# Kernel optimization log

Measured on AMD Instinct MI355X. Metric: run time of the kernel, lower is better.

The kernel has to match this reference:

```python
import jax, jax.numpy as jnp
import numpy as np

RANK = 256
ORDER = 3
B = 8192
NODES_PER = 9
NMAP = 5 ** 6          # 15625 dnn-key nodes
NDD = NMAP + 1         # + 1 device node
MDD = 2048             # edges into device node
POW5 = jnp.array([5**5, 5**4, 5**3, 5**2, 5, 1], dtype=jnp.int32)


def sage_gcn(x, src, dst, n, W, b):
    # DGL SAGEConv(aggregator='gcn'): h = fc((sum_in_neighbors + self) / (in_deg + 1))
    agg = jax.ops.segment_sum(x[src], dst, num_segments=n)
    deg = jax.ops.segment_sum(jnp.ones((src.shape[0],), x.dtype), dst, num_segments=n)
    h = (agg + x) / (deg + 1.0)[:, None]
    return h @ W + b


def layernorm(x, g, b, eps=1e-5):
    m = x.mean(-1, keepdims=True)
    v = ((x - m) ** 2).mean(-1, keepdims=True)
    return (x - m) * jax.lax.rsqrt(v + eps) * g + b


def setup_inputs() -> dict:
    key = jax.random.key(0)
    ks = jax.random.split(key, 10)
    rng = np.random.default_rng(0)
    # batched DNN graphs: B bidirectional 9-node chains
    base = np.arange(B, dtype=np.int32)[:, None] * NODES_PER
    s = (base + np.arange(NODES_PER - 1, dtype=np.int32)[None, :]).ravel()
    d = s + 1
    edge_src = jnp.asarray(np.concatenate([s, d]))
    edge_dst = jnp.asarray(np.concatenate([d, s]))
    # unique key tuples (base-5 digits of unique dnn indices)
    key_idx = rng.choice(NMAP, size=B, replace=False).astype(np.int32)
    digits = np.stack([(key_idx // 5 ** (5 - j)) % 5 for j in range(6)], axis=1)
    key_ids = jnp.asarray(digits, dtype=jnp.int32)
    features = jax.random.randint(ks[0], (B, NODES_PER), 0, 6, dtype=jnp.int32)
    dd_src = jnp.asarray(rng.choice(NMAP, size=MDD, replace=False).astype(np.int32))

    r = RANK
    def gn(k, shape, scale=0.02):
        return jax.random.normal(k, shape, jnp.float32) * scale

    return dict(
        features=features, key_ids=key_ids,
        edge_src=edge_src, edge_dst=edge_dst, dd_src=dd_src,
        emb=gn(ks[1], (6, r)),
        sage_W=gn(ks[2], (ORDER, r, r)), sage_b=jnp.zeros((ORDER, r)),
        ln_g=jnp.ones((ORDER, r)), ln_b=jnp.zeros((ORDER, r)),
        dd_W=gn(ks[3], (r, r)), dd_b=jnp.zeros((r,)),
        norm_g=jnp.ones((r,)), norm_b=jnp.zeros((r,)),
        info_W=gn(ks[4], (5, r)), info_b=jnp.zeros((r,)),
        aug_data=gn(ks[5], (1, 5), 1.0),
        pred_W1=gn(ks[6], (2 * r, r)), pred_b1=jnp.zeros((r,)),
        pred_W2=gn(ks[7], (r, 1)), pred_b2=jnp.zeros((1,)),
    )


def reference(features, key_ids, edge_src, edge_dst, dd_src,
              emb, sage_W, sage_b, ln_g, ln_b,
              dd_W, dd_b, norm_g, norm_b,
              info_W, info_b, aug_data,
              pred_W1, pred_b1, pred_W2, pred_b2):
    n = B * NODES_PER
    # GraphReader: embed + ORDER x (SAGEConv-gcn -> LayerNorm -> ReLU)
    feats = emb[features].reshape(n, RANK)
    for i in range(ORDER):
        feats = sage_gcn(feats, edge_src, edge_dst, n, sage_W[i], sage_b[i])
        feats = jax.nn.relu(layernorm(feats, ln_g[i], ln_b[i]))
    # first node of each 9-node sub-graph
    graph_embeds = feats.reshape(B, NODES_PER, RANK)[:, 0]  # [B, r]

    # scatter graph embeddings into the dnn-device graph node features
    key_idx = (key_ids * POW5).sum(axis=1)  # base-5 index from 6-tuple
    dd = jnp.zeros((NDD, RANK), feats.dtype).at[key_idx].set(graph_embeds)
    info = aug_data @ info_W + info_b  # [1, r]
    dd = dd.at[NDD - 1].set(info[0])

    # SAGEConv-gcn on the dnn-device graph (all edges point at the device node)
    dd_dst = jnp.full_like(dd_src, NDD - 1)
    dd = sage_gcn(dd, dd_src, dd_dst, NDD, dd_W, dd_b)
    dd = jax.nn.relu(layernorm(dd, norm_g, norm_b))

    info_embeds = jnp.broadcast_to(dd[-1], (B, RANK))
    embeds = jnp.concatenate([graph_embeds, info_embeds], axis=1)  # [B, 2r]
    h = jax.nn.relu(embeds @ pred_W1 + pred_b1)
    return h @ pred_W2 + pred_b2  # [B, 1]
```

## Files before the change

### kernel.cpp

```cpp
#include <hip/hip_runtime.h>

#define RANK 256
#define NB 8192
#define NMAP 15625

typedef unsigned short ushort_t;
typedef short  mfma_ab __attribute__((ext_vector_type(8)));
typedef float  f32x4   __attribute__((ext_vector_type(4)));

#define GEH_OFF   0
#define GEL_OFF   4194304
#define WTH_OFF   8388608
#define WTL_OFF   8912896
#define INV_OFF   9437184
#define PARTS_OFF 9499712
#define C2_OFF    9630784

#define DD_BLOCKS 128

__device__ __forceinline__ float b2f(ushort_t u) {
    return __uint_as_float(((unsigned)u) << 16);
}
__device__ __forceinline__ ushort_t f2b(float f) {
    unsigned u = __float_as_uint(f);
    return (ushort_t)((u + 0x7FFFu + ((u >> 16) & 1u)) >> 16);
}

__device__ __forceinline__ f32x4 mfma_bf16(mfma_ab a, mfma_ab b, f32x4 c) {
#if defined(__gfx950__)
    return __builtin_amdgcn_mfma_f32_16x16x32_bf16(a, b, c, 0, 0, 0);
#else
    (void)a; (void)b;
    return c;
#endif
}

__global__ void k_init_inv(int* inv) {
    int i = blockIdx.x * 256 + threadIdx.x;
    if (i < NMAP) inv[i] = -1;
}

__global__ void k_scatter(const int* key_ids, int* inv) {
    int b = blockIdx.x * 256 + threadIdx.x;
    const int* kp = key_ids + b * 6;
    int k = kp[0]*3125 + kp[1]*625 + kp[2]*125 + kp[3]*25 + kp[4]*5 + kp[5];
    inv[k] = b;
}

__global__ void k_prep_w(const float* __restrict__ sageW,
                         const float* __restrict__ predW1,
                         ushort_t* __restrict__ WTh,
                         ushort_t* __restrict__ WTl)
{
    const int id = blockIdx.x;
    const int mat = id >> 4, tile = id & 15;
    const int tr = tile >> 2, tc = tile & 3;
    const float* src = (mat < 3) ? (sageW + mat * 65536) : predW1;
    ushort_t* dh = WTh + mat * 65536;
    ushort_t* dl = WTl + mat * 65536;
    __shared__ float t[64][65];
    const int tid = threadIdx.x;
    const int c = tid & 63, r0 = tid >> 6;
    #pragma unroll
    for (int i = 0; i < 16; ++i) {
        int r = r0 + i * 4;
        t[r][c] = src[(tr*64 + r) * 256 + tc*64 + c];
    }
    __syncthreads();
    #pragma unroll
    for (int i = 0; i < 16; ++i) {
        int r = r0 + i * 4;
        float f = t[c][r];
        ushort_t h = f2b(f);
        dh[(tc*64 + r) * 256 + tr*64 + c] = h;
        dl[(tc*64 + r) * 256 + tr*64 + c] = f2b(f - b2f(h));
    }
}

#define GR_G 3
#define GR_RPAD 32
#define XP 260
#define AP 264

#define LN_PART(ACC0, ACC1, MT)                                                \
    _Pragma("unroll")                                                          \
    for (int q = 0; q < 4; ++q) {                                              \
        ACC0[q] += bias0; ACC1[q] += bias1;                                    \
        float s_  = ACC0[q] + ACC1[q];                                         \
        float ss_ = ACC0[q] * ACC0[q] + ACC1[q] * ACC1[q];                     \
        _Pragma("unroll")                                                      \
        for (int mask = 1; mask <= 8; mask <<= 1) {                            \
            s_  += __shfl_xor(s_, mask, 64);                                   \
            ss_ += __shfl_xor(ss_, mask, 64);                                  \
        }                                                                      \
        if (l15 == 0) sPart[(MT) * 16 + q4 * 4 + q][wid] = make_float2(s_, ss_);\
    }

#define LN_WRITE(ACC0, ACC1, MT)                                               \
    _Pragma("unroll")                                                          \
    for (int q = 0; q < 4; ++q) {                                              \
        const int row_ = (MT) * 16 + q4 * 4 + q;                               \
        if (row_ < nreal) {                                                    \
            const float2 mr_ = sMV[row_];                                      \
            float v0_ = (ACC0[q] - mr_.x) * mr_.y * gv0 + bv0;                 \
            float v1_ = (ACC1[q] - mr_.x) * mr_.y * gv1 + bv1;                 \
            v0_ = fmaxf(v0_, 0.f); v1_ = fmaxf(v1_, 0.f);                      \
            if (L < 2) {                                                       \
                sXf[row_ * XP + colb + l15]      = v0_;                        \
                sXf[row_ * XP + colb + 16 + l15] = v1_;                        \
            } else if ((row_ % 9) == 0) {                                      \
                const int gi_ = row_ / 9;                                      \
                const ushort_t h0_ = f2b(v0_), h1_ = f2b(v1_);                 \
                GEh[(b0 + gi_) * RANK + colb + l15]      = h0_;                \
                GEl[(b0 + gi_) * RANK + colb + l15]      = f2b(v0_ - b2f(h0_));\
                GEh[(b0 + gi_) * RANK + colb + 16 + l15] = h1_;                \
                GEl[(b0 + gi_) * RANK + colb + 16 + l15] = f2b(v1_ - b2f(h1_));\
            }                                                                  \
        }                                                                      \
    }

__global__ __launch_bounds__(512, 4) void k_graph_reader(
    const int* __restrict__ features,
    const float* __restrict__ emb,
    const ushort_t* __restrict__ WTh,
    const ushort_t* __restrict__ WTl,
    const float* __restrict__ sageB,
    const float* __restrict__ lnG,
    const float* __restrict__ lnB,
    ushort_t* __restrict__ GEh,
    ushort_t* __restrict__ GEl)
{
    __shared__ __align__(16) float    sXf[27 * XP];
    __shared__ __align__(16) ushort_t sAh[GR_RPAD * AP];
    __shared__ __align__(16) ushort_t sAl[GR_RPAD * AP];
    __shared__ float2 sPart[GR_RPAD][8];
    __shared__ float2 sMV[GR_RPAD];
    __shared__ int sFeat[GR_RPAD];

    const int tid  = threadIdx.x;
    const int wid  = tid >> 6;
    const int lane = tid & 63;
    const int q4   = lane >> 4;
    const int l15  = lane & 15;
    const int colb = wid * 32;

    const int b0    = blockIdx.x * GR_G;
    const int ngr   = min(GR_G, NB - b0);
    const int nreal = ngr * 9;
    const int ntask = nreal * 64;

    if (tid < GR_RPAD) sFeat[tid] = (tid < nreal) ? features[b0 * 9 + tid] : 0;
    __syncthreads();

    #pragma unroll
    for (int it = 0; it < 4; ++it) {
        int t = tid + it * 512;
        if (t < ntask) {
            int row = t >> 6, c4 = t & 63;
            *(float4*)(sXf + row * XP + c4 * 4) =
                *(const float4*)(emb + sFeat[row] * RANK + c4 * 4);
        }
    }

    const f32x4 vzero = {0.f, 0.f, 0.f, 0.f};

    for (int L = 0; L < 3; ++L) {
        float bias0, bias1, gv0, gv1, bv0, bv1;
        {
            int col0 = colb + l15, col1 = colb + 16 + l15;
            bias0 = sageB[L * RANK + col0]; bias1 = sageB[L * RANK + col1];
            gv0   = lnG[L * RANK + col0];   gv1   = lnG[L * RANK + col1];
            bv0   = lnB[L * RANK + col0];   bv1   = lnB[L * RANK + col1];
        }
        __syncthreads();

        #pragma unroll
        for (int it = 0; it < 4; ++it) {
            int t = tid + it * 512;
            if (t < ntask) {
                int row = t >> 6, c4 = t & 63;
                int j = row % 9;
                float4 v = *(const float4*)(sXf + row * XP + c4 * 4);
                float cnt = 1.f;
                if (j > 0) {
                    float4 u = *(const float4*)(sXf + (row - 1) * XP + c4 * 4);
                    v.x += u.x; v.y += u.y; v.z += u.z; v.w += u.w; cnt += 1.f;
                }
                if (j < 8) {
                    float4 u = *(const float4*)(sXf + (row + 1) * XP + c4 * 4);
                    v.x += u.x; v.y += u.y; v.z += u.z; v.w += u.w; cnt += 1.f;
                }
                float sc = 1.0f / cnt;
                v.x *= sc; v.y *= sc; v.z *= sc; v.w *= sc;
                ushort_t h0 = f2b(v.x), h1 = f2b(v.y), h2 = f2b(v.z), h3 = f2b(v.w);
                ushort_t l0 = f2b(v.x - b2f(h0)), l1 = f2b(v.y - b2f(h1));
                ushort_t l2 = f2b(v.z - b2f(h2)), l3 = f2b(v.w - b2f(h3));
                *(uint2*)(sAh + row * AP + c4 * 4) =
                    make_uint2((unsigned)h0 | ((unsigned)h1 << 16),
                               (unsigned)h2 | ((unsigned)h3 << 16));
                *(uint2*)(sAl + row * AP + c4 * 4) =
                    make_uint2((unsigned)l0 | ((unsigned)l1 << 16),
                               (unsigned)l2 | ((unsigned)l3 << 16));
            }
        }
        __syncthreads();

        f32x4 acc00 = vzero, acc01 = vzero, acc10 = vzero, acc11 = vzero;
        const ushort_t* bh = WTh + L * 65536 + (colb + l15) * RANK + q4 * 8;
        const ushort_t* bl = WTl + L * 65536 + (colb + l15) * RANK + q4 * 8;
        #pragma unroll
        for (int ks = 0; ks < 8; ++ks) {
            mfma_ab B0h = *(const mfma_ab*)(bh + ks * 32);
            mfma_ab B0l = *(const mfma_ab*)(bl + ks * 32);
            mfma_ab B1h = *(const mfma_ab*)(bh + 16 * RANK + ks * 32);
            mfma_ab B1l = *(const mfma_ab*)(bl + 16 * RANK + ks * 32);
            const int ab = l15 * AP + ks * 32 + q4 * 8;

            mfma_ab A0h = *(const mfma_ab*)(sAh + ab);
            mfma_ab A0l = *(const mfma_ab*)(sAl + ab);
            acc00 = mfma_bf16(A0h, B0h, acc00);
            acc00 = mfma_bf16(A0l, B0h, acc00);
            acc00 = mfma_bf16(A0h, B0l, acc00);
            acc01 = mfma_bf16(A0h, B1h, acc01);
            acc01 = mfma_bf16(A0l, B1h, acc01);
            acc01 = mfma_bf16(A0h, B1l, acc01);

            mfma_ab A1h = *(const mfma_ab*)(sAh + ab + 16 * AP);
            mfma_ab A1l = *(const mfma_ab*)(sAl + ab + 16 * AP);
            acc10 = mfma_bf16(A1h, B0h, acc10);
            acc10 = mfma_bf16(A1l, B0h, acc10);
            acc10 = mfma_bf16(A1h, B0l, acc10);
            acc11 = mfma_bf16(A1h, B1h, acc11);
            acc11 = mfma_bf16(A1l, B1h, acc11);
            acc11 = mfma_bf16(A1h, B1l, acc11);
        }

        LN_PART(acc00, acc01, 0)
        LN_PART(acc10, acc11, 1)
        __syncthreads();

        if (tid < GR_RPAD) {
            float s = 0.f, q = 0.f;
            #pragma unroll
            for (int w = 0; w < 8; ++w) { float2 p = sPart[tid][w]; s += p.x; q += p.y; }
            float m = s * (1.0f / 256.0f);
            float var = q * (1.0f / 256.0f) - m * m;
            if (var < 0.f) var = 0.f;
            sMV[tid] = make_float2(m, rsqrtf(var + 1e-5f));
        }
        __syncthreads();

        LN_WRITE(acc00, acc01, 0)
        LN_WRITE(acc10, acc11, 1)
    }
}

__global__ void k_dd_agg(const int* __restrict__ dd_src,
                         const int* __restrict__ inv,
                         const ushort_t* __restrict__ GEh,
                         const ushort_t* __restrict__ GEl,
                         float* __restrict__ parts)
{
    const int c  = threadIdx.x;
    const int e0 = blockIdx.x * (2048 / DD_BLOCKS);
    float s = 0.f;
    for (int e = e0; e < e0 + (2048 / DD_BLOCKS); ++e) {
        int b = inv[dd_src[e]];
        if (b >= 0) s += b2f(GEh[b * RANK + c]) + b2f(GEl[b * RANK + c]);
    }
    parts[blockIdx.x * RANK + c] = s;
}

__global__ void k_device(const float* __restrict__ parts,
                         const float* __restrict__ aug,
                         const float* __restrict__ infoW,
                         const float* __restrict__ infoB,
                         const float* __restrict__ ddW,
                         const float* __restrict__ ddB,
                         const float* __restrict__ normG,
                         const float* __restrict__ normB,
                         const float* __restrict__ predW1,
                         const float* __restrict__ predB1,
                         float* __restrict__ c2)
{
    __shared__ float sh[RANK];
    __shared__ float sdev[RANK];
    __shared__ float sred[RANK];
    const int n = threadIdx.x;

    float agg = 0.f;
    for (int p = 0; p < DD_BLOCKS; ++p) agg += parts[p * RANK + n];
    float info = infoB[n];
    for (int j = 0; j < 5; ++j) info += aug[j] * infoW[j * RANK + n];
    sh[n] = (agg + info) * (1.0f / 2049.0f);
    __syncthreads();

    float y = ddB[n];
    for (int k = 0; k < RANK; ++k) y += sh[k] * ddW[k * RANK + n];

    sred[n] = y; __syncthreads();
    for (int off = 128; off > 0; off >>= 1) {
        if (n < off) sred[n] += sred[n + off];
        __syncthreads();
    }
    float s = sred[0]; __syncthreads();
    sred[n] = y * y; __syncthreads();
    for (int off = 128; off > 0; off >>= 1) {
        if (n < off) sred[n] += sred[n + off];
        __syncthreads();
    }
    float q = sred[0]; __syncthreads();

    float m = s * (1.0f / 256.0f);
    float var = q * (1.0f / 256.0f) - m * m;
    if (var < 0.f) var = 0.f;
    float rs = rsqrtf(var + 1e-5f);
    float dev = (y - m) * rs * normG[n] + normB[n];
    if (dev < 0.f) dev = 0.f;
    sdev[n] = dev;
    __syncthreads();

    float o = predB1[n];
    for (int k = 0; k < RANK; ++k) o += sdev[k] * predW1[(RANK + k) * RANK + n];
    c2[n] = o;
}

#define PRED_MFMA3(ACC, AH, AL, BH, BL)                                        \
    ACC = mfma_bf16(AH, BH, ACC);                                              \
    ACC = mfma_bf16(AL, BH, ACC);                                              \
    ACC = mfma_bf16(AH, BL, ACC);

#define PRED_N(NT, C0, C1)                                                     \
    {                                                                          \
        mfma_ab Bh_ = *(const mfma_ab*)(bh + (NT) * 16 * RANK + ks * 32);      \
        mfma_ab Bl_ = *(const mfma_ab*)(bl + (NT) * 16 * RANK + ks * 32);      \
        PRED_MFMA3(C0, A0h, A0l, Bh_, Bl_)                                     \
        PRED_MFMA3(C1, A1h, A1l, Bh_, Bl_)                                     \
    }

#define PRED_EPI(NT, C0, C1)                                                   \
    {                                                                          \
        const int col_ = colb + (NT) * 16 + l15;                               \
        const float c2v_ = c2[col_], w2v_ = predW2[col_];                      \
        op00 += fmaxf(C0[0] + c2v_, 0.f) * w2v_;                               \
        op01 += fmaxf(C0[1] + c2v_, 0.f) * w2v_;                               \
        op02 += fmaxf(C0[2] + c2v_, 0.f) * w2v_;                               \
        op03 += fmaxf(C0[3] + c2v_, 0.f) * w2v_;                               \
        op10 += fmaxf(C1[0] + c2v_, 0.f) * w2v_;                               \
        op11 += fmaxf(C1[1] + c2v_, 0.f) * w2v_;                               \
        op12 += fmaxf(C1[2] + c2v_, 0.f) * w2v_;                               \
        op13 += fmaxf(C1[3] + c2v_, 0.f) * w2v_;                               \
    }

__global__ __launch_bounds__(128, 4) void k_pred(
    const ushort_t* __restrict__ GEh,
    const ushort_t* __restrict__ GEl,
    const ushort_t* __restrict__ W1h,
    const ushort_t* __restrict__ W1l,
    const float* __restrict__ c2,
    const float* __restrict__ predW2,
    const float* __restrict__ predB2,
    float* __restrict__ out)
{
    __shared__ float sO[2][32];
    const int tid = threadIdx.x;
    const int wid = tid >> 6;
    const int lane = tid & 63;
    const int q4 = lane >> 4, l15 = lane & 15;
    const int colb = wid * 128;
    const int m0 = blockIdx.x * 32;

    const f32x4 vzero = {0.f, 0.f, 0.f, 0.f};
    f32x4 c00 = vzero, c01 = vzero, c02 = vzero, c03 = vzero;
    f32x4 c04 = vzero, c05 = vzero, c06 = vzero, c07 = vzero;
    f32x4 c10 = vzero, c11 = vzero, c12 = vzero, c13 = vzero;
    f32x4 c14 = vzero, c15 = vzero, c16 = vzero, c17 = vzero;

    const ushort_t* ah0 = GEh + (m0 + l15) * RANK + q4 * 8;
    const ushort_t* al0 = GEl + (m0 + l15) * RANK + q4 * 8;
    const ushort_t* ah1 = ah0 + 16 * RANK;
    const ushort_t* al1 = al0 + 16 * RANK;
    const ushort_t* bh = W1h + (colb + l15) * RANK + q4 * 8;
    const ushort_t* bl = W1l + (colb + l15) * RANK + q4 * 8;

    #pragma unroll
    for (int ks = 0; ks < 8; ++ks) {
        mfma_ab A0h = *(const mfma_ab*)(ah0 + ks * 32);
        mfma_ab A0l = *(const mfma_ab*)(al0 + ks * 32);
        mfma_ab A1h = *(const mfma_ab*)(ah1 + ks * 32);
        mfma_ab A1l = *(const mfma_ab*)(al1 + ks * 32);
        PRED_N(0, c00, c10) PRED_N(1, c01, c11)
        PRED_N(2, c02, c12) PRED_N(3, c03, c13)
        PRED_N(4, c04, c14) PRED_N(5, c05, c15)
        PRED_N(6, c06, c16) PRED_N(7, c07, c17)
    }

    float op00 = 0.f, op01 = 0.f, op02 = 0.f, op03 = 0.f;
    float op10 = 0.f, op11 = 0.f, op12 = 0.f, op13 = 0.f;
    PRED_EPI(0, c00, c10) PRED_EPI(1, c01, c11)
    PRED_EPI(2, c02, c12) PRED_EPI(3, c03, c13)
    PRED_EPI(4, c04, c14) PRED_EPI(5, c05, c15)
    PRED_EPI(6, c06, c16) PRED_EPI(7, c07, c17)

    #pragma unroll
    for (int mask = 1; mask <= 8; mask <<= 1) {
        op00 += __shfl_xor(op00, mask, 64); op01 += __shfl_xor(op01, mask, 64);
        op02 += __shfl_xor(op02, mask, 64); op03 += __shfl_xor(op03, mask, 64);
        op10 += __shfl_xor(op10, mask, 64); op11 += __shfl_xor(op11, mask, 64);
        op12 += __shfl_xor(op12, mask, 64); op13 += __shfl_xor(op13, mask, 64);
    }
    if (l15 == 0) {
        sO[wid][q4 * 4 + 0] = op00; sO[wid][q4 * 4 + 1] = op01;
        sO[wid][q4 * 4 + 2] = op02; sO[wid][q4 * 4 + 3] = op03;
        sO[wid][16 + q4 * 4 + 0] = op10; sO[wid][16 + q4 * 4 + 1] = op11;
        sO[wid][16 + q4 * 4 + 2] = op12; sO[wid][16 + q4 * 4 + 3] = op13;
    }
    __syncthreads();
    if (tid < 32) out[m0 + tid] = sO[0][tid] + sO[1][tid] + predB2[0];
}

extern "C" void kernel_launch(void* const* d_in, const int* in_sizes, int n_in,
                              void* d_out, int out_size, void* d_ws, size_t ws_size,
                              hipStream_t stream) {
    const int* features  = (const int*)d_in[0];
    const int* key_ids   = (const int*)d_in[1];
    const int* dd_src    = (const int*)d_in[4];
    const float* emb     = (const float*)d_in[5];
    const float* sageW   = (const float*)d_in[6];
    const float* sageB   = (const float*)d_in[7];
    const float* lnG     = (const float*)d_in[8];
    const float* lnB     = (const float*)d_in[9];
    const float* ddW     = (const float*)d_in[10];
    const float* ddB     = (const float*)d_in[11];
    const float* normG   = (const float*)d_in[12];
    const float* normB   = (const float*)d_in[13];
    const float* infoW   = (const float*)d_in[14];
    const float* infoB   = (const float*)d_in[15];
    const float* aug     = (const float*)d_in[16];
    const float* predW1  = (const float*)d_in[17];
    const float* predB1  = (const float*)d_in[18];
    const float* predW2  = (const float*)d_in[19];
    const float* predB2  = (const float*)d_in[20];

    char* ws = (char*)d_ws;
    ushort_t* GEh   = (ushort_t*)(ws + GEH_OFF);
    ushort_t* GEl   = (ushort_t*)(ws + GEL_OFF);
    ushort_t* WTh   = (ushort_t*)(ws + WTH_OFF);
    ushort_t* WTl   = (ushort_t*)(ws + WTL_OFF);
    int*      inv   = (int*)(ws + INV_OFF);
    float*    parts = (float*)(ws + PARTS_OFF);
    float*    c2    = (float*)(ws + C2_OFF);
    float*    outp  = (float*)d_out;

    k_init_inv<<<62, 256, 0, stream>>>(inv);
    k_scatter<<<32, 256, 0, stream>>>(key_ids, inv);
    k_prep_w<<<64, 256, 0, stream>>>(sageW, predW1, WTh, WTl);
    k_graph_reader<<<(NB + GR_G - 1) / GR_G, 512, 0, stream>>>(
        features, emb, WTh, WTl, sageB, lnG, lnB, GEh, GEl);
    k_dd_agg<<<DD_BLOCKS, 256, 0, stream>>>(dd_src, inv, GEh, GEl, parts);
    k_device<<<1, 256, 0, stream>>>(parts, aug, infoW, infoB, ddW, ddB,
                                    normG, normB, predW1, predB1, c2);
    k_pred<<<NB / 32, 128, 0, stream>>>(GEh, GEl, WTh + 3 * 65536, WTl + 3 * 65536,
                                        c2, predW2, predB2, outp);
}
```

Before: 436.4 us.

## Apply neighbour aggregation after the GEMM via register shuffles, pack 5 graphs per block

Uses linearity to reorder the SAGE layer: the 256x256 matmul is applied to the raw features and the 3-point chain stencil (mean of self and neighbours) is then applied to the MFMA accumulators through cross-lane shuffles. This removes the separate shared-memory stencil pass, its fp32 staging buffer and one barrier per layer. Block size grows from 3 to 5 graphs (45 rows padded to 48, three 16-row M tiles) so each B-fragment load feeds more MFMAs, and B fragments are prefetched one k-step ahead. The bf16 hi/lo split is now applied before the stencil, so rounding behaviour changes slightly, and per-thread register pressure rises.

```diff
diff --git a/kernel.cpp b/kernel.cpp
--- a/kernel.cpp
+++ b/kernel.cpp
@@ -33,6 +33,14 @@
     (void)a; (void)b;
     return c;
 #endif
+}
+
+__device__ __forceinline__ float sten1(float x, float up, float dn, int R) {
+    int j = R % 9;
+    float fu = (j != 0) ? 1.f : 0.f;
+    float fd = (j != 8) ? 1.f : 0.f;
+    float sc = (fu + fd > 1.5f) ? (1.f / 3.f) : 0.5f;
+    return (x + fu * up + fd * dn) * sc;
 }
 
 __global__ void k_init_inv(int* inv) {
@@ -77,9 +85,9 @@
     }
 }
 
-#define GR_G 3
-#define GR_RPAD 32
-#define XP 260
+#define GR_G 5
+#define GR_ROWS 45
+#define GR_RPAD 48
 #define AP 264
 
 #define LN_PART(ACC0, ACC1, MT)                                                \
@@ -93,7 +101,9 @@
             s_  += __shfl_xor(s_, mask, 64);                                   \
             ss_ += __shfl_xor(ss_, mask, 64);                                  \
         }                                                                      \
-        if (l15 == 0) sPart[(MT) * 16 + q4 * 4 + q][wid] = make_float2(s_, ss_);\
+        const int prow_ = (MT) * 16 + q4 * 4 + q;                              \
+        if (l15 == 0 && prow_ < GR_ROWS)                                       \
+            sPart[prow_][wid] = make_float2(s_, ss_);                          \
     }
 
 #define LN_WRITE(ACC0, ACC1, MT)                                               \
@@ -105,18 +115,55 @@
             float v0_ = (ACC0[q] - mr_.x) * mr_.y * gv0 + bv0;                 \
             float v1_ = (ACC1[q] - mr_.x) * mr_.y * gv1 + bv1;                 \
             v0_ = fmaxf(v0_, 0.f); v1_ = fmaxf(v1_, 0.f);                      \
+            const ushort_t h0_ = f2b(v0_), h1_ = f2b(v1_);                     \
+            const ushort_t lo0_ = f2b(v0_ - b2f(h0_));                         \
+            const ushort_t lo1_ = f2b(v1_ - b2f(h1_));                         \
             if (L < 2) {                                                       \
-                sXf[row_ * XP + colb + l15]      = v0_;                        \
-                sXf[row_ * XP + colb + 16 + l15] = v1_;                        \
+                sXh[row_ * AP + colb + l15]      = h0_;                        \
+                sXl[row_ * AP + colb + l15]      = lo0_;                       \
+                sXh[row_ * AP + colb + 16 + l15] = h1_;                        \
+                sXl[row_ * AP + colb + 16 + l15] = lo1_;                       \
             } else if ((row_ % 9) == 0) {                                      \
                 const int gi_ = row_ / 9;                                      \
-                const ushort_t h0_ = f2b(v0_), h1_ = f2b(v1_);                 \
                 GEh[(b0 + gi_) * RANK + colb + l15]      = h0_;                \
-                GEl[(b0 + gi_) * RANK + colb + l15]      = f2b(v0_ - b2f(h0_));\
+                GEl[(b0 + gi_) * RANK + colb + l15]      = lo0_;               \
                 GEh[(b0 + gi_) * RANK + colb + 16 + l15] = h1_;                \
-                GEl[(b0 + gi_) * RANK + colb + 16 + l15] = f2b(v1_ - b2f(h1_));\
+                GEl[(b0 + gi_) * RANK + colb + 16 + l15] = lo1_;               \
             }                                                                  \
         }                                                                      \
+    }
+
+#define STENCIL_COL(V0, V1, V2)                                                \
+    {                                                                          \
+        float ui0 = __shfl(V0[3], lane - 16), di0 = __shfl(V0[0], lane + 16);  \
+        float ui1 = __shfl(V1[3], lane - 16), di1 = __shfl(V1[0], lane + 16);  \
+        float ui2 = __shfl(V2[3], lane - 16), di2 = __shfl(V2[0], lane + 16);  \
+        float xu1 = __shfl(V0[3], l15 + 48);       \
+        float xu2 = __shfl(V1[3], l15 + 48);       \
+        float xd0 = __shfl(V1[0], l15);           \
+        float xd1 = __shfl(V2[0], l15);           \
+        const int rb0 = q4 * 4, rb1 = 16 + q4 * 4, rb2 = 32 + q4 * 4;          \
+        float u0 = (q4 == 0) ? 0.f : ui0;                                      \
+        float d0 = (q4 == 3) ? xd0 : di0;                                      \
+        float u1 = (q4 == 0) ? xu1 : ui1;                                      \
+        float d1 = (q4 == 3) ? xd1 : di1;                                      \
+        float u2 = (q4 == 0) ? xu2 : ui2;                                      \
+        float d2 = (q4 == 3) ? 0.f : di2;                                      \
+        float z00 = sten1(V0[0], u0,    V0[1], rb0 + 0);                       \
+        float z01 = sten1(V0[1], V0[0], V0[2], rb0 + 1);                       \
+        float z02 = sten1(V0[2], V0[1], V0[3], rb0 + 2);                       \
+        float z03 = sten1(V0[3], V0[2], d0,    rb0 + 3);                       \
+        float z10 = sten1(V1[0], u1,    V1[1], rb1 + 0);                       \
+        float z11 = sten1(V1[1], V1[0], V1[2], rb1 + 1);                       \
+        float z12 = sten1(V1[2], V1[1], V1[3], rb1 + 2);                       \
+        float z13 = sten1(V1[3], V1[2], d1,    rb1 + 3);                       \
+        float z20 = sten1(V2[0], u2,    V2[1], rb2 + 0);                       \
+        float z21 = sten1(V2[1], V2[0], V2[2], rb2 + 1);                       \
+        float z22 = sten1(V2[2], V2[1], V2[3], rb2 + 2);                       \
+        float z23 = sten1(V2[3], V2[2], d2,    rb2 + 3);                       \
+        V0[0] = z00; V0[1] = z01; V0[2] = z02; V0[3] = z03;                    \
+        V1[0] = z10; V1[1] = z11; V1[2] = z12; V1[3] = z13;                    \
+        V2[0] = z20; V2[1] = z21; V2[2] = z22; V2[3] = z23;                    \
     }
 
 __global__ __launch_bounds__(512, 4) void k_graph_reader(
@@ -130,12 +177,11 @@
     ushort_t* __restrict__ GEh,
     ushort_t* __restrict__ GEl)
 {
-    __shared__ __align__(16) float    sXf[27 * XP];
-    __shared__ __align__(16) ushort_t sAh[GR_RPAD * AP];
-    __shared__ __align__(16) ushort_t sAl[GR_RPAD * AP];
-    __shared__ float2 sPart[GR_RPAD][8];
-    __shared__ float2 sMV[GR_RPAD];
-    __shared__ int sFeat[GR_RPAD];
+    __shared__ __align__(16) ushort_t sXh[GR_RPAD * AP];
+    __shared__ __align__(16) ushort_t sXl[GR_RPAD * AP];
+    __shared__ float2 sPart[GR_ROWS][8];
+    __shared__ float2 sMV[GR_ROWS];
+    __shared__ int sFeat[GR_ROWS];
 
     const int tid  = threadIdx.x;
     const int wid  = tid >> 6;
@@ -147,19 +193,26 @@
     const int b0    = blockIdx.x * GR_G;
     const int ngr   = min(GR_G, NB - b0);
     const int nreal = ngr * 9;
-    const int ntask = nreal * 64;
-
-    if (tid < GR_RPAD) sFeat[tid] = (tid < nreal) ? features[b0 * 9 + tid] : 0;
+
+    if (tid < GR_ROWS) sFeat[tid] = (tid < nreal) ? features[b0 * 9 + tid] : 0;
     __syncthreads();
 
     #pragma unroll
-    for (int it = 0; it < 4; ++it) {
+    for (int it = 0; it < 6; ++it) {
         int t = tid + it * 512;
-        if (t < ntask) {
-            int row = t >> 6, c4 = t & 63;
-            *(float4*)(sXf + row * XP + c4 * 4) =
-                *(const float4*)(emb + sFeat[row] * RANK + c4 * 4);
-        }
+        int row = t >> 6, c4 = t & 63;
+        float4 v = make_float4(0.f, 0.f, 0.f, 0.f);
+        if (row < nreal)
+            v = *(const float4*)(emb + sFeat[row] * RANK + c4 * 4);
+        ushort_t h0 = f2b(v.x), h1 = f2b(v.y), h2 = f2b(v.z), h3 = f2b(v.w);
+        ushort_t l0 = f2b(v.x - b2f(h0)), l1 = f2b(v.y - b2f(h1));
+        ushort_t l2 = f2b(v.z - b2f(h2)), l3 = f2b(v.w - b2f(h3));
+        *(uint2*)(sXh + row * AP + c4 * 4) =
+            make_uint2((unsigned)h0 | ((unsigned)h1 << 16),
+                       (unsigned)h2 | ((unsigned)h3 << 16));
+        *(uint2*)(sXl + row * AP + c4 * 4) =
+            make_uint2((unsigned)l0 | ((unsigned)l1 << 16),
+                       (unsigned)l2 | ((unsigned)l3 << 16));
     }
 
     const f32x4 vzero = {0.f, 0.f, 0.f, 0.f};
@@ -174,72 +227,65 @@
         }
         __syncthreads();
 
-        #pragma unroll
-        for (int it = 0; it < 4; ++it) {
-            int t = tid + it * 512;
-            if (t < ntask) {
-                int row = t >> 6, c4 = t & 63;
-                int j = row % 9;
-                float4 v = *(const float4*)(sXf + row * XP + c4 * 4);
-                float cnt = 1.f;
-                if (j > 0) {
-                    float4 u = *(const float4*)(sXf + (row - 1) * XP + c4 * 4);
-                    v.x += u.x; v.y += u.y; v.z += u.z; v.w += u.w; cnt += 1.f;
-                }
-                if (j < 8) {
-                    float4 u = *(const float4*)(sXf + (row + 1) * XP + c4 * 4);
-                    v.x += u.x; v.y += u.y; v.z += u.z; v.w += u.w; cnt += 1.f;
-                }
-                float sc = 1.0f / cnt;
-                v.x *= sc; v.y *= sc; v.z *= sc; v.w *= sc;
-                ushort_t h0 = f2b(v.x), h1 = f2b(v.y), h2 = f2b(v.z), h3 = f2b(v.w);
-                ushort_t l0 = f2b(v.x - b2f(h0)), l1 = f2b(v.y - b2f(h1));
-                ushort_t l2 = f2b(v.z - b2f(h2)), l3 = f2b(v.w - b2f(h3));
-                *(uint2*)(sAh + row * AP + c4 * 4) =
-                    make_uint2((unsigned)h0 | ((unsigned)h1 << 16),
-                               (unsigned)h2 | ((unsigned)h3 << 16));
-                *(uint2*)(sAl + row * AP + c4 * 4) =
-                    make_uint2((unsigned)l0 | ((unsigned)l1 << 16),
-                               (unsigned)l2 | ((unsigned)l3 << 16));
-            }
-        }
-        __syncthreads();
-
-        f32x4 acc00 = vzero, acc01 = vzero, acc10 = vzero, acc11 = vzero;
+        f32x4 a00 = vzero, a01 = vzero;
+        f32x4 a10 = vzero, a11 = vzero;
+        f32x4 a20 = vzero, a21 = vzero;
         const ushort_t* bh = WTh + L * 65536 + (colb + l15) * RANK + q4 * 8;
         const ushort_t* bl = WTl + L * 65536 + (colb + l15) * RANK + q4 * 8;
+        mfma_ab B0h = *(const mfma_ab*)(bh);
+        mfma_ab B0l = *(const mfma_ab*)(bl);
+        mfma_ab B1h = *(const mfma_ab*)(bh + 16 * RANK);
+        mfma_ab B1l = *(const mfma_ab*)(bl + 16 * RANK);
         #pragma unroll
         for (int ks = 0; ks < 8; ++ks) {
-            mfma_ab B0h = *(const mfma_ab*)(bh + ks * 32);
-            mfma_ab B0l = *(const mfma_ab*)(bl + ks * 32);
-            mfma_ab B1h = *(const mfma_ab*)(bh + 16 * RANK + ks * 32);
-            mfma_ab B1l = *(const mfma_ab*)(bl + 16 * RANK + ks * 32);
+            mfma_ab nB0h, nB0l, nB1h, nB1l;
+            if (ks < 7) {
+                nB0h = *(const mfma_ab*)(bh + (ks + 1) * 32);
+                nB0l = *(const mfma_ab*)(bl + (ks + 1) * 32);
+                nB1h = *(const mfma_ab*)(bh + 16 * RANK + (ks + 1) * 32);
+                nB1l = *(const mfma_ab*)(bl + 16 * RANK + (ks + 1) * 32);
+            }
             const int ab = l15 * AP + ks * 32 + q4 * 8;
 
-            mfma_ab A0h = *(const mfma_ab*)(sAh + ab);
-            mfma_ab A0l = *(const mfma_ab*)(sAl + ab);
-            acc00 = mfma_bf16(A0h, B0h, acc00);
-            acc00 = mfma_bf16(A0l, B0h, acc00);
-            acc00 = mfma_bf16(A0h, B0l, acc00);
-            acc01 = mfma_bf16(A0h, B1h, acc01);
-            acc01 = mfma_bf16(A0l, B1h, acc01);
-            acc01 = mfma_bf16(A0h, B1l, acc01);
-
-            mfma_ab A1h = *(const mfma_ab*)(sAh + ab + 16 * AP);
-            mfma_ab A1l = *(const mfma_ab*)(sAl + ab + 16 * AP);
-            acc10 = mfma_bf16(A1h, B0h, acc10);
-            acc10 = mfma_bf16(A1l, B0h, acc10);
-            acc10 = mfma_bf16(A1h, B0l, acc10);
-            acc11 = mfma_bf16(A1h, B1h, acc11);
-            acc11 = mfma_bf16(A1l, B1h, acc11);
-            acc11 = mfma_bf16(A1h, B1l, acc11);
+            mfma_ab Ah = *(const mfma_ab*)(sXh + ab);
+            mfma_ab Al = *(const mfma_ab*)(sXl + ab);
+            a00 = mfma_bf16(Ah, B0h, a00);
+            a00 = mfma_bf16(Al, B0h, a00);
+            a00 = mfma_bf16(Ah, B0l, a00);
+            a01 = mfma_bf16(Ah, B1h, a01);
+            a01 = mfma_bf16(Al, B1h, a01);
+            a01 = mfma_bf16(Ah, B1l, a01);
+
+            Ah = *(const mfma_ab*)(sXh + ab + 16 * AP);
+            Al = *(const mfma_ab*)(sXl + ab + 16 * AP);
+            a10 = mfma_bf16(Ah, B0h, a10);
+            a10 = mfma_bf16(Al, B0h, a10);
+            a10 = mfma_bf16(Ah, B0l, a10);
+            a11 = mfma_bf16(Ah, B1h, a11);
+            a11 = mfma_bf16(Al, B1h, a11);
+            a11 = mfma_bf16(Ah, B1l, a11);
+
+            Ah = *(const mfma_ab*)(sXh + ab + 32 * AP);
+            Al = *(const mfma_ab*)(sXl + ab + 32 * AP);
+            a20 = mfma_bf16(Ah, B0h, a20);
+            a20 = mfma_bf16(Al, B0h, a20);
+            a20 = mfma_bf16(Ah, B0l, a20);
+            a21 = mfma_bf16(Ah, B1h, a21);
+            a21 = mfma_bf16(Al, B1h, a21);
+            a21 = mfma_bf16(Ah, B1l, a21);
+
+            if (ks < 7) { B0h = nB0h; B0l = nB0l; B1h = nB1h; B1l = nB1l; }
         }
 
-        LN_PART(acc00, acc01, 0)
-        LN_PART(acc10, acc11, 1)
+        STENCIL_COL(a00, a10, a20)
+        STENCIL_COL(a01, a11, a21)
+
+        LN_PART(a00, a01, 0)
+        LN_PART(a10, a11, 1)
+        LN_PART(a20, a21, 2)
         __syncthreads();
 
-        if (tid < GR_RPAD) {
+        if (tid < GR_ROWS) {
             float s = 0.f, q = 0.f;
             #pragma unroll
             for (int w = 0; w < 8; ++w) { float2 p = sPart[tid][w]; s += p.x; q += p.y; }
@@ -250,8 +296,9 @@
         }
         __syncthreads();
 
-        LN_WRITE(acc00, acc01, 0)
-        LN_WRITE(acc10, acc11, 1)
+        LN_WRITE(a00, a01, 0)
+        LN_WRITE(a10, a11, 1)
+        LN_WRITE(a20, a21, 2)
     }
 }
 
```

New measurement: 442.0 us. No clear change (+1.3%).
